# Performance work log

Measured on AMD Instinct MI355X. Metric: run time of the kernel, lower is better.

The kernel has to match this reference:

```python
import jax, jax.numpy as jnp
import numpy as np

B, H, W, C = 16, 32, 32, 512
NUM_HEADS = 8
ATTN_DIM = 512
HEAD_DIM = ATTN_DIM // NUM_HEADS
EPS = 1e-5


def setup_inputs() -> dict:
    key = jax.random.key(0)
    ks = jax.random.split(key, 6)
    s_in = 1.0 / np.sqrt(C)
    s_attn = 1.0 / np.sqrt(ATTN_DIM)
    return {
        "x": jax.random.normal(ks[0], (B, H, W, C), dtype=jnp.float32),
        "gamma": jnp.ones((C,), dtype=jnp.float32),
        "beta": jnp.zeros((C,), dtype=jnp.float32),
        "wq": jax.random.normal(ks[1], (C, ATTN_DIM), dtype=jnp.float32) * s_in,
        "bq": jnp.zeros((ATTN_DIM,), dtype=jnp.float32),
        "wk": jax.random.normal(ks[2], (C, ATTN_DIM), dtype=jnp.float32) * s_in,
        "bk": jnp.zeros((ATTN_DIM,), dtype=jnp.float32),
        "wv": jax.random.normal(ks[3], (C, ATTN_DIM), dtype=jnp.float32) * s_in,
        "bv": jnp.zeros((ATTN_DIM,), dtype=jnp.float32),
        "wo": jax.random.normal(ks[4], (ATTN_DIM, C), dtype=jnp.float32) * s_attn,
        "bo": jnp.zeros((C,), dtype=jnp.float32),
    }


def reference(x, gamma, beta, wq, bq, wk, bk, wv, bv, wo, bo):
    b, h, w, c = x.shape
    t = h * w  # number of spatial tokens
    # GroupNorm with 1 group: normalize over (H, W, C) per sample
    mean = jnp.mean(x, axis=(1, 2, 3), keepdims=True)
    var = jnp.var(x, axis=(1, 2, 3), keepdims=True)
    xn = (x - mean) * jax.lax.rsqrt(var + EPS) * gamma + beta
    xn = xn.reshape(b, t, c)
    # 1x1-conv q/k/v == dense over channel dim; split into heads
    q = (xn @ wq + bq).reshape(b, t, NUM_HEADS, HEAD_DIM)
    k = (xn @ wk + bk).reshape(b, t, NUM_HEADS, HEAD_DIM)
    v = (xn @ wv + bv).reshape(b, t, NUM_HEADS, HEAD_DIM)
    scale = 1.0 / jnp.sqrt(jnp.asarray(HEAD_DIM, dtype=x.dtype))
    scores = jnp.einsum('bqhd,bkhd->bhqk', q, k) * scale
    probs = jax.nn.softmax(scores, axis=-1)
    attn = jnp.einsum('bhqk,bkhd->bqhd', probs, v).reshape(b, t, ATTN_DIM)
    out = attn @ wo + bo
    # Multiplex([None, branch]): residual add, then Reshape([-1, model_dim])
    return x.reshape(b, t, c) + out
```

## Files before the change

### kernel.cpp

```cpp
#include <hip/hip_runtime.h>
#include <hip/hip_bf16.h>

typedef __attribute__((ext_vector_type(8))) short short8;
typedef __attribute__((ext_vector_type(4))) short short4v;
typedef __attribute__((ext_vector_type(4))) float f32x4;

#define B_ 16
#define T_ 1024
#define C_ 512
#define NH 8
#define HD 64

__device__ __forceinline__ short f2bf(float f) {
  union { float f; unsigned u; } v;
  v.f = f;
  unsigned r = v.u + 0x7fffu + ((v.u >> 16) & 1u);
  return (short)(r >> 16);
}

__device__ __forceinline__ short2 pack_bf2(float a, float b) {
  __hip_bfloat162 t = __float22bfloat162_rn(make_float2(a, b));
  short2 r;
  __builtin_memcpy(&r, &t, 4);
  return r;
}

__device__ __forceinline__ void gload_lds16(const short* g, short* l) {
  __builtin_amdgcn_global_load_lds(
      (const __attribute__((address_space(1))) void*)g,
      (__attribute__((address_space(3))) void*)l, 16, 0, 0);
}

__global__ __launch_bounds__(256) void stats1_kernel(const float* __restrict__ x,
                                                     float2* __restrict__ partials) {
  int chunk = blockIdx.x;
  int b = blockIdx.y;
  int tid = threadIdx.x;
  const float4* xb = (const float4*)(x + (size_t)b * 524288 + (size_t)chunk * 8192);
  float s = 0.f, s2 = 0.f;
#pragma unroll
  for (int i = 0; i < 8; i++) {
    float4 v = xb[tid + i * 256];
    s  += v.x + v.y + v.z + v.w;
    s2 += v.x * v.x + v.y * v.y + v.z * v.z + v.w * v.w;
  }
  __shared__ float ls[256], ls2[256];
  ls[tid] = s; ls2[tid] = s2;
  __syncthreads();
  for (int o = 128; o > 0; o >>= 1) {
    if (tid < o) { ls[tid] += ls[tid + o]; ls2[tid] += ls2[tid + o]; }
    __syncthreads();
  }
  if (tid == 0) partials[b * 64 + chunk] = make_float2(ls[0], ls2[0]);
}

__global__ __launch_bounds__(64) void stats2_kernel(const float2* __restrict__ partials,
                                                    float* __restrict__ stats) {
  int b = blockIdx.x;
  float2 p = partials[b * 64 + threadIdx.x];
  float s = p.x, s2 = p.y;
#pragma unroll
  for (int off = 1; off < 64; off <<= 1) {
    s  += __shfl_xor(s,  off, 64);
    s2 += __shfl_xor(s2, off, 64);
  }
  if (threadIdx.x == 0) {
    float mean = s * (1.f / 524288.f);
    float var  = s2 * (1.f / 524288.f) - mean * mean;
    stats[b * 2]     = mean;
    stats[b * 2 + 1] = rsqrtf(var + 1e-5f);
  }
}

__global__ __launch_bounds__(256) void norm_kernel(const float* __restrict__ x,
                                                   const float* __restrict__ gamma,
                                                   const float* __restrict__ beta,
                                                   const float* __restrict__ stats,
                                                   short* __restrict__ xn) {
  size_t i4 = (size_t)blockIdx.x * 256 + threadIdx.x;
  float4 v = ((const float4*)x)[i4];
  size_t i = i4 * 4;
  int b = (int)(i >> 19);
  int c = (int)(i & 511);
  float mean = stats[b * 2], rstd = stats[b * 2 + 1];
  short4v o;
  o[0] = f2bf((v.x - mean) * rstd * gamma[c + 0] + beta[c + 0]);
  o[1] = f2bf((v.y - mean) * rstd * gamma[c + 1] + beta[c + 1]);
  o[2] = f2bf((v.z - mean) * rstd * gamma[c + 2] + beta[c + 2]);
  o[3] = f2bf((v.w - mean) * rstd * gamma[c + 3] + beta[c + 3]);
  ((short4v*)xn)[i4] = o;
}

__global__ __launch_bounds__(256) void transpose_w_all(const float* __restrict__ wq,
                                                       const float* __restrict__ wk,
                                                       const float* __restrict__ wv,
                                                       const float* __restrict__ wo,
                                                       short* __restrict__ wqkvT,
                                                       short* __restrict__ woT) {
  int o = blockIdx.x * 256 + threadIdx.x;
  int sel = o >> 18;
  int oo = o & 262143;
  int k = oo >> 9, n = oo & 511;
  const float* w = (sel == 0) ? wq : (sel == 1) ? wk : (sel == 2) ? wv : wo;
  float val = w[oo];
  if (sel < 3) wqkvT[((size_t)(sel * 512 + n)) * 512 + k] = f2bf(val);
  else         woT[(size_t)n * 512 + k] = f2bf(val);
}

__global__ __launch_bounds__(256) void gemm_qkv(const short* __restrict__ A,
                                                const short* __restrict__ Bt,
                                                const float* __restrict__ bq,
                                                const float* __restrict__ bk,
                                                const float* __restrict__ bv,
                                                short* __restrict__ C) {
  __shared__ __align__(16) short As[128 * 32];
  __shared__ __align__(16) short Bs[128 * 32];
  int tid = threadIdx.x;
  int w = tid >> 6, lane = tid & 63;
  int quad = lane >> 4, l16 = lane & 15;
  int mw = (w >> 1) * 64, nw = (w & 1) * 64;
  int seg = (blockIdx.x * 128) >> 9;
  const float* bias = (seg == 0) ? bq : (seg == 1) ? bk : bv;
  float smul = (seg == 0) ? 0.125f : 1.0f;
  const short* Atile = A + (size_t)(blockIdx.y * 128) * 512;
  const short* Btile = Bt + (size_t)(blockIdx.x * 128) * 512;
  int srow = (w << 4) + (lane >> 2);
  int scol = (lane & 3) * 8;
  f32x4 acc[4][4] = {};
  for (int k0 = 0; k0 < 512; k0 += 32) {
    __syncthreads();
    gload_lds16(&Atile[(size_t)srow * 512 + k0 + scol],        &As[w * 512]);
    gload_lds16(&Atile[(size_t)(srow + 64) * 512 + k0 + scol], &As[2048 + w * 512]);
    gload_lds16(&Btile[(size_t)srow * 512 + k0 + scol],        &Bs[w * 512]);
    gload_lds16(&Btile[(size_t)(srow + 64) * 512 + k0 + scol], &Bs[2048 + w * 512]);
    __syncthreads();
    short8 af[4], bf[4];
#pragma unroll
    for (int i = 0; i < 4; i++) af[i] = *(const short8*)(&As[(mw + i * 16 + l16) * 32 + quad * 8]);
#pragma unroll
    for (int i = 0; i < 4; i++) bf[i] = *(const short8*)(&Bs[(nw + i * 16 + l16) * 32 + quad * 8]);
#pragma unroll
    for (int mi = 0; mi < 4; mi++)
#pragma unroll
      for (int ni = 0; ni < 4; ni++)
        acc[mi][ni] = __builtin_amdgcn_mfma_f32_16x16x32_bf16(af[mi], bf[ni], acc[mi][ni], 0, 0, 0);
  }
  int m0 = blockIdx.y * 128 + mw;
  int n0 = blockIdx.x * 128 + nw;
#pragma unroll
  for (int mi = 0; mi < 4; mi++)
#pragma unroll
    for (int ni = 0; ni < 4; ni++) {
      int col = n0 + ni * 16 + l16;
      float bval = bias[col & 511];
#pragma unroll
      for (int r = 0; r < 4; r++) {
        int row = m0 + mi * 16 + quad * 4 + r;
        C[(size_t)row * 1536 + col] = f2bf((acc[mi][ni][r] + bval) * smul);
      }
    }
}

__global__ __launch_bounds__(256) void gemm_out(const short* __restrict__ A,
                                                const short* __restrict__ Bt,
                                                const float* __restrict__ bias,
                                                const float* __restrict__ xres,
                                                float* __restrict__ out) {
  __shared__ __align__(16) short As[128 * 32];
  __shared__ __align__(16) short Bs[128 * 32];
  int tid = threadIdx.x;
  int w = tid >> 6, lane = tid & 63;
  int quad = lane >> 4, l16 = lane & 15;
  int mw = (w >> 1) * 64, nw = (w & 1) * 64;
  const short* Atile = A + (size_t)(blockIdx.y * 128) * 512;
  const short* Btile = Bt + (size_t)(blockIdx.x * 128) * 512;
  int srow = (w << 4) + (lane >> 2);
  int scol = (lane & 3) * 8;
  f32x4 acc[4][4] = {};
  for (int k0 = 0; k0 < 512; k0 += 32) {
    __syncthreads();
    gload_lds16(&Atile[(size_t)srow * 512 + k0 + scol],        &As[w * 512]);
    gload_lds16(&Atile[(size_t)(srow + 64) * 512 + k0 + scol], &As[2048 + w * 512]);
    gload_lds16(&Btile[(size_t)srow * 512 + k0 + scol],        &Bs[w * 512]);
    gload_lds16(&Btile[(size_t)(srow + 64) * 512 + k0 + scol], &Bs[2048 + w * 512]);
    __syncthreads();
    short8 af[4], bf[4];
#pragma unroll
    for (int i = 0; i < 4; i++) af[i] = *(const short8*)(&As[(mw + i * 16 + l16) * 32 + quad * 8]);
#pragma unroll
    for (int i = 0; i < 4; i++) bf[i] = *(const short8*)(&Bs[(nw + i * 16 + l16) * 32 + quad * 8]);
#pragma unroll
    for (int mi = 0; mi < 4; mi++)
#pragma unroll
      for (int ni = 0; ni < 4; ni++)
        acc[mi][ni] = __builtin_amdgcn_mfma_f32_16x16x32_bf16(af[mi], bf[ni], acc[mi][ni], 0, 0, 0);
  }
  int m0 = blockIdx.y * 128 + mw;
  int n0 = blockIdx.x * 128 + nw;
#pragma unroll
  for (int mi = 0; mi < 4; mi++)
#pragma unroll
    for (int ni = 0; ni < 4; ni++) {
      int col = n0 + ni * 16 + l16;
      float bval = bias[col];
#pragma unroll
      for (int r = 0; r < 4; r++) {
        int row = m0 + mi * 16 + quad * 4 + r;
        out[(size_t)row * 512 + col] = acc[mi][ni][r] + bval + xres[(size_t)row * 512 + col];
      }
    }
}

__global__ __launch_bounds__(256) void vtrans_kernel(const short* __restrict__ qkv,
                                                     short* __restrict__ vT) {
  int tt = blockIdx.x;
  int h  = blockIdx.y;
  int b  = blockIdx.z;
  int tid = threadIdx.x;
  __shared__ short TB[64 * 72];
  const short* src = qkv + ((size_t)b * T_) * 1536 + 1024 + (size_t)h * 64;
#pragma unroll
  for (int i = 0; i < 2; i++) {
    int idx = tid + i * 256;
    int t = idx >> 3, c = idx & 7;
    short8 vv = *(const short8*)(src + (size_t)(tt * 64 + t) * 1536 + c * 8);
    *(short8*)(&TB[t * 72 + c * 8]) = vv;
  }
  __syncthreads();
  short* dst = vT + (((size_t)b * NH + h) * HD) * T_ + tt * 64;
#pragma unroll
  for (int i = 0; i < 2; i++) {
    int idx = tid + i * 256;
    int d = idx >> 3, c = idx & 7;
    short8 o;
#pragma unroll
    for (int j = 0; j < 8; j++) o[j] = TB[(c * 8 + j) * 72 + d];
    *(short8*)(dst + (size_t)d * T_ + c * 8) = o;
  }
}

__global__ __launch_bounds__(256) void attn_kernel(const short* __restrict__ Q,
                                                   const short* __restrict__ Kmat,
                                                   const short* __restrict__ vT,
                                                   short* __restrict__ O) {
  int tid = threadIdx.x;
  int w = tid >> 6, lane = tid & 63;
  int quad = lane >> 4, l16 = lane & 15;
  int bh = blockIdx.x;
  int qt = blockIdx.y;
  int b = bh >> 3, h = bh & 7;
  size_t base  = ((size_t)b * T_) * 1536 + (size_t)h * 64;
  size_t vbase = (((size_t)b * NH + h) * HD) * T_;
  size_t obase = ((size_t)b * T_) * 512 + (size_t)h * 64;
  int qrow0 = qt * 64;

  __shared__ __align__(16) char smem[128 * 72 * 2 + 64 * 132 * 2 + 256 * 4];
  short* KT = (short*)smem;
  short* VT = (short*)(smem + 128 * 72 * 2);
  float* Lbuf = (float*)smem;
  float* denomL = (float*)(smem + 128 * 72 * 2 + 64 * 132 * 2);

  short8 qf0[4], qf1[4];
#pragma unroll
  for (int g = 0; g < 4; g++) {
    const short* qp = Q + base + (size_t)(qrow0 + g * 16 + l16) * 1536 + quad * 8;
    qf0[g] = *(const short8*)qp;
    qf1[g] = *(const short8*)(qp + 32);
  }

  f32x4 oacc[4][4] = {};
  float lsum[4] = {0.f, 0.f, 0.f, 0.f};

  for (int kk0 = 0; kk0 < T_; kk0 += 128) {
    __syncthreads();
#pragma unroll
    for (int i = 0; i < 4; i++) {
      int idx = tid + i * 256;
      int r0 = idx >> 3, c = idx & 7;
      *(short8*)(&KT[r0 * 72 + c * 8]) =
          *(const short8*)(Kmat + base + (size_t)(kk0 + r0) * 1536 + c * 8);
    }
#pragma unroll
    for (int i = 0; i < 4; i++) {
      int idx = tid + i * 256;
      int d = idx >> 4, c16 = idx & 15;
      *(short8*)(&VT[d * 132 + c16 * 8]) =
          *(const short8*)(vT + vbase + (size_t)d * 1024 + kk0 + c16 * 8);
    }
    __syncthreads();

    int ra = w * 16;
    short8 kfa0 = *(const short8*)(&KT[(ra + l16) * 72 + quad * 8]);
    short8 kfa1 = *(const short8*)(&KT[(ra + l16) * 72 + quad * 8 + 32]);
    short8 kfb0 = *(const short8*)(&KT[(ra + 64 + l16) * 72 + quad * 8]);
    short8 kfb1 = *(const short8*)(&KT[(ra + 64 + l16) * 72 + quad * 8 + 32]);
    short8 vf[4];
#pragma unroll
    for (int f = 0; f < 4; f++) {
      const short* vp = &VT[(f * 16 + l16) * 132];
      short4v va = *(const short4v*)(vp + ra + quad * 4);
      short4v vb = *(const short4v*)(vp + ra + 64 + quad * 4);
      short8 t;
      t[0] = va[0]; t[1] = va[1]; t[2] = va[2]; t[3] = va[3];
      t[4] = vb[0]; t[5] = vb[1]; t[6] = vb[2]; t[7] = vb[3];
      vf[f] = t;
    }
#pragma unroll
    for (int g = 0; g < 4; g++) {
      f32x4 za = {}, zb = {};
      za = __builtin_amdgcn_mfma_f32_16x16x32_bf16(kfa0, qf0[g], za, 0, 0, 0);
      za = __builtin_amdgcn_mfma_f32_16x16x32_bf16(kfa1, qf1[g], za, 0, 0, 0);
      zb = __builtin_amdgcn_mfma_f32_16x16x32_bf16(kfb0, qf0[g], zb, 0, 0, 0);
      zb = __builtin_amdgcn_mfma_f32_16x16x32_bf16(kfb1, qf1[g], zb, 0, 0, 0);
      float pa0 = __expf(za[0]), pa1 = __expf(za[1]);
      float pa2 = __expf(za[2]), pa3 = __expf(za[3]);
      float pb0 = __expf(zb[0]), pb1 = __expf(zb[1]);
      float pb2 = __expf(zb[2]), pb3 = __expf(zb[3]);
      lsum[g] += (pa0 + pa1) + (pa2 + pa3) + (pb0 + pb1) + (pb2 + pb3);
      short2 a01 = pack_bf2(pa0, pa1), a23 = pack_bf2(pa2, pa3);
      short2 b01 = pack_bf2(pb0, pb1), b23 = pack_bf2(pb2, pb3);
      short8 pf;
      pf[0] = a01.x; pf[1] = a01.y; pf[2] = a23.x; pf[3] = a23.y;
      pf[4] = b01.x; pf[5] = b01.y; pf[6] = b23.x; pf[7] = b23.y;
#pragma unroll
      for (int f = 0; f < 4; f++)
        oacc[f][g] = __builtin_amdgcn_mfma_f32_16x16x32_bf16(vf[f], pf, oacc[f][g], 0, 0, 0);
    }
  }

#pragma unroll
  for (int g = 0; g < 4; g++) {
    lsum[g] += __shfl_xor(lsum[g], 16, 64);
    lsum[g] += __shfl_xor(lsum[g], 32, 64);
  }
  if (quad == 0) {
#pragma unroll
    for (int g = 0; g < 4; g++) denomL[w * 64 + g * 16 + l16] = lsum[g];
  }
  for (int ww = 0; ww < 4; ww++) {
    __syncthreads();
    if (w == ww) {
#pragma unroll
      for (int g = 0; g < 4; g++)
#pragma unroll
        for (int f = 0; f < 4; f++) {
          float* p = &Lbuf[(g * 16 + l16) * 68 + f * 16 + quad * 4];
          if (ww == 0) *(f32x4*)p = oacc[f][g];
          else         *(f32x4*)p = *(f32x4*)p + oacc[f][g];
        }
    }
  }
  __syncthreads();

  int q = tid >> 2, seg = tid & 3;
  float dn = denomL[q] + denomL[64 + q] + denomL[128 + q] + denomL[192 + q];
  float rinv = __frcp_rn(dn);
  const float* row = &Lbuf[q * 68 + seg * 16];
  short8 o0, o1;
#pragma unroll
  for (int i = 0; i < 8; i++) o0[i] = f2bf(row[i] * rinv);
#pragma unroll
  for (int i = 0; i < 8; i++) o1[i] = f2bf(row[8 + i] * rinv);
  short* op = O + obase + (size_t)(qrow0 + q) * 512 + seg * 16;
  *(short8*)op = o0;
  *(short8*)(op + 8) = o1;
}

extern "C" void kernel_launch(void* const* d_in, const int* in_sizes, int n_in,
                              void* d_out, int out_size, void* d_ws, size_t ws_size,
                              hipStream_t stream) {
  const float* x     = (const float*)d_in[0];
  const float* gamma = (const float*)d_in[1];
  const float* beta  = (const float*)d_in[2];
  const float* wq    = (const float*)d_in[3];
  const float* bq    = (const float*)d_in[4];
  const float* wk    = (const float*)d_in[5];
  const float* bk    = (const float*)d_in[6];
  const float* wv    = (const float*)d_in[7];
  const float* bv    = (const float*)d_in[8];
  const float* wo    = (const float*)d_in[9];
  const float* bo    = (const float*)d_in[10];
  float* out = (float*)d_out;

  char* ws = (char*)d_ws;
  const size_t XN_ELEMS = (size_t)B_ * T_ * C_;
  size_t off = 0;
  float* stats = (float*)(ws + off); off += 256;
  float2* partials = (float2*)(ws + off); off += 16 * 64 * sizeof(float2);
  short* xn    = (short*)(ws + off); off += XN_ELEMS * 2;
  short* wqkvT = (short*)(ws + off); off += (size_t)1536 * 512 * 2;
  short* woT   = (short*)(ws + off); off += (size_t)512 * 512 * 2;
  short* qkv   = (short*)(ws + off); off += (size_t)B_ * T_ * 1536 * 2;
  short* vTb   = (short*)(ws + off); off += XN_ELEMS * 2;
  short* ao    = (short*)(ws + off); off += XN_ELEMS * 2;

  stats1_kernel<<<dim3(64, 16), 256, 0, stream>>>(x, partials);
  stats2_kernel<<<16, 64, 0, stream>>>(partials, stats);
  norm_kernel<<<8192, 256, 0, stream>>>(x, gamma, beta, stats, xn);
  transpose_w_all<<<4096, 256, 0, stream>>>(wq, wk, wv, wo, wqkvT, woT);

  gemm_qkv<<<dim3(12, 128), 256, 0, stream>>>(xn, wqkvT, bq, bk, bv, qkv);

  vtrans_kernel<<<dim3(16, 8, 16), 256, 0, stream>>>(qkv, vTb);
  attn_kernel<<<dim3(128, 16), 256, 0, stream>>>(qkv, qkv + 512, vTb, ao);

  gemm_out<<<dim3(4, 128), 256, 0, stream>>>(ao, woT, bo, x, out);
}
```

Measured before the change: 259.7 us.

## Load K/V tiles via direct global-to-LDS with XOR swizzle in attention

The attention kernel now stages K and V tiles using direct global-to-LDS loads (gload_lds16) into XOR-swizzled, unpadded shared memory instead of register round-trips. The V transpose kernel is reorganized to emit a pre-permuted layout so each lane reads its V MFMA fragment as one 16-byte load rather than two 8-byte loads plus repacking. Launch bounds add an occupancy hint of 4 blocks per CU. The goal is to cut VGPR pressure and LDS traffic and to avoid bank conflicts, at the cost of coupling the vtrans layout tightly to the attention fragment order.

```diff
diff --git a/kernel.cpp b/kernel.cpp
--- a/kernel.cpp
+++ b/kernel.cpp
@@ -213,36 +213,39 @@
 
 __global__ __launch_bounds__(256) void vtrans_kernel(const short* __restrict__ qkv,
                                                      short* __restrict__ vT) {
-  int tt = blockIdx.x;
+  int chunk = blockIdx.x;
   int h  = blockIdx.y;
   int b  = blockIdx.z;
   int tid = threadIdx.x;
-  __shared__ short TB[64 * 72];
-  const short* src = qkv + ((size_t)b * T_) * 1536 + 1024 + (size_t)h * 64;
-#pragma unroll
-  for (int i = 0; i < 2; i++) {
+  __shared__ short TB[128 * 72];
+  const short* src = qkv + ((size_t)b * T_ + chunk * 128) * 1536 + 1024 + (size_t)h * 64;
+#pragma unroll
+  for (int i = 0; i < 4; i++) {
     int idx = tid + i * 256;
     int t = idx >> 3, c = idx & 7;
-    short8 vv = *(const short8*)(src + (size_t)(tt * 64 + t) * 1536 + c * 8);
-    *(short8*)(&TB[t * 72 + c * 8]) = vv;
+    *(short8*)(&TB[t * 72 + c * 8]) = *(const short8*)(src + (size_t)t * 1536 + c * 8);
   }
   __syncthreads();
-  short* dst = vT + (((size_t)b * NH + h) * HD) * T_ + tt * 64;
-#pragma unroll
-  for (int i = 0; i < 2; i++) {
+  short* dst = vT + ((size_t)(b * 8 + h) * 64) * 1024 + chunk * 128;
+#pragma unroll
+  for (int i = 0; i < 4; i++) {
     int idx = tid + i * 256;
-    int d = idx >> 3, c = idx & 7;
+    int d = idx >> 4, sc = idx & 15;
+    int w2 = sc >> 2, q2 = sc & 3;
     short8 o;
 #pragma unroll
-    for (int j = 0; j < 8; j++) o[j] = TB[(c * 8 + j) * 72 + d];
-    *(short8*)(dst + (size_t)d * T_ + c * 8) = o;
-  }
-}
-
-__global__ __launch_bounds__(256) void attn_kernel(const short* __restrict__ Q,
-                                                   const short* __restrict__ Kmat,
-                                                   const short* __restrict__ vT,
-                                                   short* __restrict__ O) {
+    for (int sg = 0; sg < 8; sg++) {
+      int half = sg >> 2, r = sg & 3;
+      o[sg] = TB[(half * 64 + w2 * 16 + q2 * 4 + r) * 72 + d];
+    }
+    *(short8*)(dst + (size_t)d * 1024 + sc * 8) = o;
+  }
+}
+
+__global__ __launch_bounds__(256, 4) void attn_kernel(const short* __restrict__ Q,
+                                                      const short* __restrict__ Kmat,
+                                                      const short* __restrict__ vTg,
+                                                      short* __restrict__ O) {
   int tid = threadIdx.x;
   int w = tid >> 6, lane = tid & 63;
   int quad = lane >> 4, l16 = lane & 15;
@@ -250,15 +253,15 @@
   int qt = blockIdx.y;
   int b = bh >> 3, h = bh & 7;
   size_t base  = ((size_t)b * T_) * 1536 + (size_t)h * 64;
-  size_t vbase = (((size_t)b * NH + h) * HD) * T_;
+  size_t vbase = ((size_t)bh * 64) * 1024;
   size_t obase = ((size_t)b * T_) * 512 + (size_t)h * 64;
   int qrow0 = qt * 64;
 
-  __shared__ __align__(16) char smem[128 * 72 * 2 + 64 * 132 * 2 + 256 * 4];
+  __shared__ __align__(16) char smem[32768 + 1024];
   short* KT = (short*)smem;
-  short* VT = (short*)(smem + 128 * 72 * 2);
+  short* VT = (short*)(smem + 16384);
   float* Lbuf = (float*)smem;
-  float* denomL = (float*)(smem + 128 * 72 * 2 + 64 * 132 * 2);
+  float* denomL = (float*)(smem + 32768);
 
   short8 qf0[4], qf1[4];
 #pragma unroll
@@ -268,43 +271,47 @@
     qf1[g] = *(const short8*)(qp + 32);
   }
 
+  const short* ksrc[4];
+  const short* vsrc[4];
+#pragma unroll
+  for (int n = 0; n < 4; n++) {
+    int bk = w * 256 + n * 64 + lane;
+    int key = bk >> 3, jc = bk & 7;
+    int dcol = jc ^ (key & 7);
+    ksrc[n] = Kmat + base + (size_t)key * 1536 + dcol * 8;
+    int d = bk >> 4, j = bk & 15;
+    int kc = j ^ (d & 15);
+    vsrc[n] = vTg + vbase + (size_t)d * 1024 + kc * 8;
+  }
+
+  int l7 = l16 & 7;
+  int kA0 = ((w * 16 + l16) * 8 + (quad ^ l7)) * 8;
+  int kA1 = ((w * 16 + l16) * 8 + ((quad + 4) ^ l7)) * 8;
+  int kB0 = kA0 + 4096;
+  int kB1 = kA1 + 4096;
+  int vOff = (l16 * 16 + ((w * 4 + quad) ^ l16)) * 8;
+
   f32x4 oacc[4][4] = {};
   float lsum[4] = {0.f, 0.f, 0.f, 0.f};
 
   for (int kk0 = 0; kk0 < T_; kk0 += 128) {
     __syncthreads();
 #pragma unroll
-    for (int i = 0; i < 4; i++) {
-      int idx = tid + i * 256;
-      int r0 = idx >> 3, c = idx & 7;
-      *(short8*)(&KT[r0 * 72 + c * 8]) =
-          *(const short8*)(Kmat + base + (size_t)(kk0 + r0) * 1536 + c * 8);
-    }
-#pragma unroll
-    for (int i = 0; i < 4; i++) {
-      int idx = tid + i * 256;
-      int d = idx >> 4, c16 = idx & 15;
-      *(short8*)(&VT[d * 132 + c16 * 8]) =
-          *(const short8*)(vT + vbase + (size_t)d * 1024 + kk0 + c16 * 8);
-    }
-    __syncthreads();
-
-    int ra = w * 16;
-    short8 kfa0 = *(const short8*)(&KT[(ra + l16) * 72 + quad * 8]);
-    short8 kfa1 = *(const short8*)(&KT[(ra + l16) * 72 + quad * 8 + 32]);
-    short8 kfb0 = *(const short8*)(&KT[(ra + 64 + l16) * 72 + quad * 8]);
-    short8 kfb1 = *(const short8*)(&KT[(ra + 64 + l16) * 72 + quad * 8 + 32]);
-    short8 vf[4];
-#pragma unroll
-    for (int f = 0; f < 4; f++) {
-      const short* vp = &VT[(f * 16 + l16) * 132];
-      short4v va = *(const short4v*)(vp + ra + quad * 4);
-      short4v vb = *(const short4v*)(vp + ra + 64 + quad * 4);
-      short8 t;
-      t[0] = va[0]; t[1] = va[1]; t[2] = va[2]; t[3] = va[3];
-      t[4] = vb[0]; t[5] = vb[1]; t[6] = vb[2]; t[7] = vb[3];
-      vf[f] = t;
-    }
+    for (int n = 0; n < 4; n++)
+      gload_lds16(ksrc[n] + (size_t)kk0 * 1536, KT + (w * 256 + n * 64) * 8);
+#pragma unroll
+    for (int n = 0; n < 4; n++)
+      gload_lds16(vsrc[n] + kk0, VT + (w * 256 + n * 64) * 8);
+    __syncthreads();
+
+    short8 kfa0 = *(const short8*)(KT + kA0);
+    short8 kfa1 = *(const short8*)(KT + kA1);
+    short8 kfb0 = *(const short8*)(KT + kB0);
+    short8 kfb1 = *(const short8*)(KT + kB1);
+    short8 vfr[4];
+#pragma unroll
+    for (int f = 0; f < 4; f++) vfr[f] = *(const short8*)(VT + vOff + f * 2048);
+
 #pragma unroll
     for (int g = 0; g < 4; g++) {
       f32x4 za = {}, zb = {};
@@ -324,7 +331,7 @@
       pf[4] = b01.x; pf[5] = b01.y; pf[6] = b23.x; pf[7] = b23.y;
 #pragma unroll
       for (int f = 0; f < 4; f++)
-        oacc[f][g] = __builtin_amdgcn_mfma_f32_16x16x32_bf16(vf[f], pf, oacc[f][g], 0, 0, 0);
+        oacc[f][g] = __builtin_amdgcn_mfma_f32_16x16x32_bf16(vfr[f], pf, oacc[f][g], 0, 0, 0);
     }
   }
 
@@ -401,7 +408,7 @@
 
   gemm_qkv<<<dim3(12, 128), 256, 0, stream>>>(xn, wqkvT, bq, bk, bv, qkv);
 
-  vtrans_kernel<<<dim3(16, 8, 16), 256, 0, stream>>>(qkv, vTb);
+  vtrans_kernel<<<dim3(8, 8, 16), 256, 0, stream>>>(qkv, vTb);
   attn_kernel<<<dim3(128, 16), 256, 0, stream>>>(qkv, qkv + 512, vTb, ao);
 
   gemm_out<<<dim3(4, 128), 256, 0, stream>>>(ao, woT, bo, x, out);
```

New measurement: 461.6 us. 1.78x slower.
